# Kernel optimization log

Hardware: AMD Instinct MI355X
Metric: run time of the kernel (lower is better)

Reference implementation:

```python
import jax, jax.numpy as jnp
import numpy as np

TONECURVE_LENGTH = 256
RESOLUTION = 1024  # tone_curve_resolution
B, H, W = 8, 1024, 1536

RANGES = {
    'Temperature': (2000.0, 50000.0),
    'Tint': (-150.0, 150.0),
    'Exposure2012': (-5.0, 5.0),
    'Contrast2012': (-100.0, 100.0),
    'Highlights2012': (-100.0, 100.0),
    'Shadows2012': (-100.0, 100.0),
    'Whites2012': (-100.0, 100.0),
    'Blacks2012': (-100.0, 100.0),
    'Vibrance': (-100.0, 100.0),
    'Saturation': (-100.0, 100.0),
}

def _denorm(name, v):
    lo, hi = RANGES[name]
    return lo + 0.5 * (v + 1.0) * (hi - lo)

def _luminance(img):
    return 0.2126 * img[:, 0:1] + 0.7152 * img[:, 1:2] + 0.0722 * img[:, 2:3]

def _white_balance(img, temperature, tint):
    temp = jnp.clip(temperature, 2000.0, 50000.0)
    tr = 6500.0 / temp
    red = jnp.sqrt(tr)
    blue = 1.0 / jnp.sqrt(tr)
    ts = jnp.clip(tint / 150.0, -1.5, 1.5)
    green = 1.0 - 0.1 * ts
    red = red * (1.0 + 0.05 * ts)
    blue = blue * (1.0 - 0.05 * ts)
    gains = jnp.stack([red, green, blue], axis=1)[:, :, None, None]  # [B,3,1,1]
    balanced = img * gains
    norm = jnp.max(gains, axis=1, keepdims=True)
    return jnp.clip(balanced / jnp.maximum(norm, 1e-4), 0.0, 4.0)

def _region(img, luma, value, pivot, width):
    strength = (value / 100.0)[:, None, None, None]
    mask = jax.nn.sigmoid((luma - pivot) / width)
    mask = mask - jnp.mean(mask, axis=(2, 3), keepdims=True)
    new_luma = jnp.clip(luma + strength * mask, 0.0, 1.0)
    ratio = jnp.where(luma > 1e-4, new_luma / jnp.maximum(luma, 1e-4), 1.0)
    return jnp.clip(img * ratio, 0.0, 1.0), new_luma

def _tone_curve(img, tone_curve):
    luma = jnp.clip(_luminance(img), 0.0, 1.0)  # [B,1,H,W]
    # linear interp of [B,L] control points to [B,RESOLUTION], align_corners=True
    src = jnp.arange(RESOLUTION, dtype=jnp.float32) * ((TONECURVE_LENGTH - 1) / (RESOLUTION - 1))
    i0 = jnp.floor(src).astype(jnp.int32)
    i1 = jnp.minimum(i0 + 1, TONECURVE_LENGTH - 1)
    w = src - i0.astype(jnp.float32)
    curve = tone_curve[:, i0] * (1.0 - w) + tone_curve[:, i1] * w  # [B,RESOLUTION]
    coords = luma * (RESOLUTION - 1)
    idx_low = jnp.floor(coords).astype(jnp.int32)
    idx_high = jnp.minimum(idx_low + 1, RESOLUTION - 1)
    weight = coords - idx_low.astype(jnp.float32)
    b = img.shape[0]
    g_low = jnp.take_along_axis(curve, idx_low.reshape(b, -1), axis=1).reshape(luma.shape)
    g_high = jnp.take_along_axis(curve, idx_high.reshape(b, -1), axis=1).reshape(luma.shape)
    target = (1.0 - weight) * g_low + weight * g_high
    ratio = jnp.where(luma > 1e-5, target / jnp.maximum(luma, 1e-5), 1.0)
    return jnp.clip(img * ratio, 0.0, 1.0)

def _vibrance(img, vibrance):
    luma = _luminance(img)
    chroma = img - luma
    cn = jnp.sqrt(jnp.sum(chroma * chroma, axis=1, keepdims=True) + 1e-6)
    mask = jnp.exp(-4.0 * cn)
    gain = jnp.clip(1.0 + (vibrance / 100.0)[:, None, None, None] * mask, 0.2, 4.0)
    return jnp.clip(luma + chroma * gain, 0.0, 1.0)

def _saturation(img, saturation):
    luma = _luminance(img)
    chroma = img - luma
    gain = (1.0 + saturation / 100.0)[:, None, None, None]
    return jnp.clip(luma + chroma * gain, 0.0, 1.0)


def setup_inputs() -> dict:
    key = jax.random.key(0)
    ks = jax.random.split(key, 12)
    sliders = {}
    names = ['temperature_n', 'tint_n', 'exposure_n', 'contrast_n', 'highlights_n',
             'shadows_n', 'whites_n', 'blacks_n', 'vibrance_n', 'saturation_n']
    for i, n in enumerate(names):
        sliders[n] = jax.random.uniform(ks[i], (B,), jnp.float32, -1.0, 1.0)
    image = jax.random.uniform(ks[10], (B, 3, H, W), jnp.float32)
    tone_curve = jnp.sort(jax.random.uniform(ks[11], (B, TONECURVE_LENGTH), jnp.float32), axis=1)
    return {'image': image, 'tone_curve': tone_curve, **sliders}


def reference(image, tone_curve, temperature_n, tint_n, exposure_n, contrast_n,
              highlights_n, shadows_n, whites_n, blacks_n, vibrance_n, saturation_n):
    img = jnp.clip(image, 0.0, 1.0)
    temperature = _denorm('Temperature', temperature_n)
    tint = _denorm('Tint', tint_n)
    exposure = _denorm('Exposure2012', exposure_n)
    contrast = _denorm('Contrast2012', contrast_n)
    highlights = _denorm('Highlights2012', highlights_n)
    shadows = _denorm('Shadows2012', shadows_n)
    whites = _denorm('Whites2012', whites_n)
    blacks = _denorm('Blacks2012', blacks_n)
    vibrance = _denorm('Vibrance', vibrance_n)
    saturation = _denorm('Saturation', saturation_n)

    img = _white_balance(img, temperature, tint)
    img = img * jnp.power(2.0, exposure)[:, None, None, None]  # exposure
    img = jnp.clip(img, 0.0, 4.0)
    factor = (1.0 + contrast / 100.0)[:, None, None, None]      # contrast
    img = jnp.clip((img - 0.5) * factor + 0.5, 0.0, 1.0)

    luma = jnp.clip(_luminance(img), 0.0, 1.0)
    img, luma = _region(img, luma, highlights, 0.7, 0.1)
    img, luma = _region(img, luma, shadows, 0.3, 0.12)
    img, luma = _region(img, luma, whites, 0.9, 0.08)
    img, luma = _region(img, luma, blacks, 0.1, 0.08)

    img = _tone_curve(img, tone_curve)
    img = _vibrance(img, vibrance)
    img = _saturation(img, saturation)
    return jnp.clip(img, 0.0, 1.0)
```

## Files before the change

### kernel.cpp

```cpp
#include <hip/hip_runtime.h>
#include <math.h>

#define H_DIM 1024
#define W_DIM 1536
#define HW_PIX (H_DIM * W_DIM)
#define NBATCH 8
#define QPB (HW_PIX / 4)
#define RBPB 192
#define QPT_R (QPB / (RBPB * 256))
#define FQPT 4
#define FBPB (QPB / (256 * FQPT))
#define RESOLUTION 1024
#define TC_LEN 256

typedef float vfloat4 __attribute__((ext_vector_type(4)));

struct Sliders {
    const float* temperature; const float* tint; const float* exposure; const float* contrast;
    const float* highlights;  const float* shadows; const float* whites; const float* blacks;
    const float* vibrance;    const float* saturation;
};

__device__ __forceinline__ float denorm(float v, float lo, float hi) {
    return lo + 0.5f * (v + 1.0f) * (hi - lo);
}
__device__ __forceinline__ float clamp01(float x) {
    return __builtin_amdgcn_fmed3f(x, 0.f, 1.f);
}
__device__ __forceinline__ float clampf(float x, float lo, float hi) {
    return fminf(fmaxf(x, lo), hi);
}
__device__ __forceinline__ float sigmoidf(float x) {
    float t = __builtin_amdgcn_exp2f(x * -1.4426950408889634f);
    return __builtin_amdgcn_rcpf(1.0f + t);
}

struct FrontP { float sr, sg, sb, em, cf; };

__device__ __forceinline__ FrontP front_params(const Sliders& S, int b) {
    float temp = clampf(denorm(S.temperature[b], 2000.f, 50000.f), 2000.f, 50000.f);
    float tr   = 6500.f / temp;
    float red  = sqrtf(tr);
    float blue = 1.0f / sqrtf(tr);
    float ts   = clampf(denorm(S.tint[b], -150.f, 150.f) * (1.0f / 150.0f), -1.5f, 1.5f);
    float green = 1.0f - 0.1f * ts;
    red  *= (1.0f + 0.05f * ts);
    blue *= (1.0f - 0.05f * ts);
    float norm = fmaxf(fmaxf(red, green), blue);
    float inv  = 1.0f / fmaxf(norm, 1e-4f);
    FrontP p;
    p.sr = red * inv; p.sg = green * inv; p.sb = blue * inv;
    p.em = exp2f(denorm(S.exposure[b], -5.f, 5.f));
    p.cf = 1.0f + denorm(S.contrast[b], -100.f, 100.f) * 0.01f;
    return p;
}

__device__ __forceinline__ float front_chan(float x, float s, float em, float cf) {
    x = clamp01(x);
    x = x * s;
    x = fminf(x * em, 4.0f);
    return clamp01((x - 0.5f) * cf + 0.5f);
}

__device__ __forceinline__ float luminance(float r, float g, float b) {
    return 0.2126f * r + 0.7152f * g + 0.0722f * b;
}

__device__ __forceinline__ double block_sum_d(double v) {
    #pragma unroll
    for (int o = 32; o > 0; o >>= 1) v += __shfl_down(v, o, 64);
    __shared__ double s[4];
    int lane = threadIdx.x & 63, wid = threadIdx.x >> 6;
    if (lane == 0) s[wid] = v;
    __syncthreads();
    double r = 0.0;
    if (threadIdx.x == 0) r = s[0] + s[1] + s[2] + s[3];
    return r;
}

__device__ __forceinline__ float partial_mean(const double* __restrict__ ws_part, int k, int b) {
    const double* pp = ws_part + (k * NBATCH + b) * RBPB;
    double v = (threadIdx.x < RBPB) ? pp[threadIdx.x] : 0.0;
    double t = block_sum_d(v);
    __shared__ float sh;
    if (threadIdx.x == 0) sh = (float)(t * (1.0 / (double)HW_PIX));
    __syncthreads();
    float m = sh;
    __syncthreads();
    return m;
}

__device__ __forceinline__ void build_curve(float* curve, const float* tone_curve, int b) {
    const float* tc = tone_curve + b * TC_LEN;
    for (int j = threadIdx.x; j < RESOLUTION; j += 256) {
        float src = (float)j * ((float)(TC_LEN - 1) / (float)(RESOLUTION - 1));
        float fi  = floorf(src);
        int   i0  = (int)fi;
        int   i1  = min(i0 + 1, TC_LEN - 1);
        float w   = src - fi;
        curve[j]  = tc[i0] * (1.0f - w) + tc[i1] * w;
    }
}

template <int R, bool USE_LUMA>
__global__ __launch_bounds__(256)
void reduce_kernel(const float* __restrict__ image, Sliders S,
                   float* __restrict__ ws_luma, double* __restrict__ ws_part) {
    const int b   = blockIdx.x / RBPB;
    const int blk = blockIdx.x % RBPB;

    const float pivots[4] = {0.7f, 0.3f, 0.9f, 0.1f};
    const float invw[4]   = {1.0f / 0.1f, 1.0f / 0.12f, 1.0f / 0.08f, 1.0f / 0.08f};
    const float* sliders[4] = {S.highlights, S.shadows, S.whites, S.blacks};

    float strength[4], meanv[4];
    #pragma unroll
    for (int k = 0; k < R; k++) {
        strength[k] = denorm(sliders[k][b], -100.f, 100.f) * 0.01f;
        meanv[k]    = partial_mean(ws_part, k, b);
    }
    FrontP p = front_params(S, b);

    double sum = 0.0;
    #pragma unroll
    for (int it = 0; it < QPT_R; it++) {
        const int q   = blk * (256 * QPT_R) + it * 256 + threadIdx.x;
        const int off = q * 4;

        float4 L;
        if (USE_LUMA && R > 0) {
            L = *reinterpret_cast<const float4*>(ws_luma + (size_t)b * HW_PIX + off);
        } else {
            const float* base = image + (size_t)b * 3 * HW_PIX + off;
            float4 r4 = *reinterpret_cast<const float4*>(base);
            float4 g4 = *reinterpret_cast<const float4*>(base + HW_PIX);
            float4 b4 = *reinterpret_cast<const float4*>(base + 2 * HW_PIX);
            float* rr = reinterpret_cast<float*>(&r4);
            float* gg = reinterpret_cast<float*>(&g4);
            float* bb = reinterpret_cast<float*>(&b4);
            float* ll = reinterpret_cast<float*>(&L);
            #pragma unroll
            for (int i = 0; i < 4; i++) {
                float r  = front_chan(rr[i], p.sr, p.em, p.cf);
                float g  = front_chan(gg[i], p.sg, p.em, p.cf);
                float bl = front_chan(bb[i], p.sb, p.em, p.cf);
                ll[i] = clamp01(luminance(r, g, bl));
            }
            if (USE_LUMA && R == 0)
                *reinterpret_cast<float4*>(ws_luma + (size_t)b * HW_PIX + off) = L;
        }

        const float* ll = reinterpret_cast<const float*>(&L);
        #pragma unroll
        for (int i = 0; i < 4; i++) {
            float lum = ll[i];
            #pragma unroll
            for (int k = 0; k < R; k++) {
                float mask = sigmoidf((lum - pivots[k]) * invw[k]);
                lum = clamp01(lum + strength[k] * (mask - meanv[k]));
            }
            sum += (double)sigmoidf((lum - pivots[R]) * invw[R]);
        }
    }
    sum = block_sum_d(sum);
    if (threadIdx.x == 0) ws_part[(R * NBATCH + b) * RBPB + blk] = sum;
}

__global__ __launch_bounds__(256)
void final_kernel(const float* __restrict__ image, const float* __restrict__ tone_curve,
                  Sliders S, const double* __restrict__ ws_part, float* __restrict__ out) {
    const int b   = blockIdx.x / FBPB;
    const int blk = blockIdx.x % FBPB;

    __shared__ float curve[RESOLUTION];
    build_curve(curve, tone_curve, b);

    const float pivots[4] = {0.7f, 0.3f, 0.9f, 0.1f};
    const float invw[4]   = {1.0f / 0.1f, 1.0f / 0.12f, 1.0f / 0.08f, 1.0f / 0.08f};
    const float* sliders[4] = {S.highlights, S.shadows, S.whites, S.blacks};

    FrontP p = front_params(S, b);
    float strength[4], meanv[4];
    #pragma unroll
    for (int k = 0; k < 4; k++) {
        strength[k] = denorm(sliders[k][b], -100.f, 100.f) * 0.01f;
        meanv[k]    = partial_mean(ws_part, k, b);
    }
    float vib  = denorm(S.vibrance[b],   -100.f, 100.f) * 0.01f;
    float satg = 1.0f + denorm(S.saturation[b], -100.f, 100.f) * 0.01f;

    for (int it = 0; it < FQPT; it++) {
        const int q   = blk * (256 * FQPT) + it * 256 + threadIdx.x;
        const int off = q * 4;

        const float* base = image + (size_t)b * 3 * HW_PIX + off;
        float4 r4 = *reinterpret_cast<const float4*>(base);
        float4 g4 = *reinterpret_cast<const float4*>(base + HW_PIX);
        float4 b4 = *reinterpret_cast<const float4*>(base + 2 * HW_PIX);
        float* rr = reinterpret_cast<float*>(&r4);
        float* gg = reinterpret_cast<float*>(&g4);
        float* bb = reinterpret_cast<float*>(&b4);

        #pragma unroll
        for (int i = 0; i < 4; i++) {
            float r  = front_chan(rr[i], p.sr, p.em, p.cf);
            float g  = front_chan(gg[i], p.sg, p.em, p.cf);
            float bl = front_chan(bb[i], p.sb, p.em, p.cf);
            float lum = clamp01(luminance(r, g, bl));

            #pragma unroll
            for (int k = 0; k < 4; k++) {
                float mask = sigmoidf((lum - pivots[k]) * invw[k]);
                float nl   = clamp01(lum + strength[k] * (mask - meanv[k]));
                float ratio = (lum > 1e-4f) ? nl * __builtin_amdgcn_rcpf(lum) : 1.0f;
                r  = fminf(r * ratio, 1.f);
                g  = fminf(g * ratio, 1.f);
                bl = fminf(bl * ratio, 1.f);
                lum = nl;
            }

            float tl = clamp01(luminance(r, g, bl));
            float coords = tl * (float)(RESOLUTION - 1);
            float fidx = floorf(coords);
            int   i0 = (int)fidx;
            int   i1 = min(i0 + 1, RESOLUTION - 1);
            float w  = coords - fidx;
            float target = (1.0f - w) * curve[i0] + w * curve[i1];
            float ratio  = (tl > 1e-5f) ? target * __builtin_amdgcn_rcpf(tl) : 1.0f;
            r  = fminf(r * ratio, 1.f);
            g  = fminf(g * ratio, 1.f);
            bl = fminf(bl * ratio, 1.f);

            float l2 = luminance(r, g, bl);
            float cr = r - l2, cg = g - l2, cb = bl - l2;
            float cn = sqrtf(cr * cr + cg * cg + cb * cb + 1e-6f);
            float gmask = __builtin_amdgcn_exp2f(cn * -5.771f);
            float vg = __builtin_amdgcn_fmed3f(1.0f + vib * gmask, 0.2f, 4.0f);
            r  = clamp01(l2 + cr * vg);
            g  = clamp01(l2 + cg * vg);
            bl = clamp01(l2 + cb * vg);

            float l3 = luminance(r, g, bl);
            r  = clamp01(l3 + (r - l3) * satg);
            g  = clamp01(l3 + (g - l3) * satg);
            bl = clamp01(l3 + (bl - l3) * satg);

            rr[i] = r; gg[i] = g; bb[i] = bl;
        }

        float* op = out + (size_t)b * 3 * HW_PIX + off;
        __builtin_nontemporal_store(*reinterpret_cast<vfloat4*>(&r4),
                                    reinterpret_cast<vfloat4*>(op));
        __builtin_nontemporal_store(*reinterpret_cast<vfloat4*>(&g4),
                                    reinterpret_cast<vfloat4*>(op + HW_PIX));
        __builtin_nontemporal_store(*reinterpret_cast<vfloat4*>(&b4),
                                    reinterpret_cast<vfloat4*>(op + 2 * HW_PIX));
    }
}

extern "C" void kernel_launch(void* const* d_in, const int* in_sizes, int n_in,
                              void* d_out, int out_size, void* d_ws, size_t ws_size,
                              hipStream_t stream) {
    const float* image      = (const float*)d_in[0];
    const float* tone_curve = (const float*)d_in[1];
    Sliders S;
    S.temperature = (const float*)d_in[2];
    S.tint        = (const float*)d_in[3];
    S.exposure    = (const float*)d_in[4];
    S.contrast    = (const float*)d_in[5];
    S.highlights  = (const float*)d_in[6];
    S.shadows     = (const float*)d_in[7];
    S.whites      = (const float*)d_in[8];
    S.blacks      = (const float*)d_in[9];
    S.vibrance    = (const float*)d_in[10];
    S.saturation  = (const float*)d_in[11];
    float* out = (float*)d_out;

    double* ws_part = (double*)d_ws;
    float*  ws_luma = (float*)((char*)d_ws + 4 * NBATCH * RBPB * sizeof(double) + 256);
    bool use_luma = ws_size >= 4 * NBATCH * RBPB * sizeof(double) + 256
                              + (size_t)NBATCH * HW_PIX * sizeof(float);

    dim3 rgrid(NBATCH * RBPB), block(256);
    if (use_luma) {
        reduce_kernel<0, true><<<rgrid, block, 0, stream>>>(image, S, ws_luma, ws_part);
        reduce_kernel<1, true><<<rgrid, block, 0, stream>>>(image, S, ws_luma, ws_part);
        reduce_kernel<2, true><<<rgrid, block, 0, stream>>>(image, S, ws_luma, ws_part);
        reduce_kernel<3, true><<<rgrid, block, 0, stream>>>(image, S, ws_luma, ws_part);
    } else {
        reduce_kernel<0, false><<<rgrid, block, 0, stream>>>(image, S, ws_luma, ws_part);
        reduce_kernel<1, false><<<rgrid, block, 0, stream>>>(image, S, ws_luma, ws_part);
        reduce_kernel<2, false><<<rgrid, block, 0, stream>>>(image, S, ws_luma, ws_part);
        reduce_kernel<3, false><<<rgrid, block, 0, stream>>>(image, S, ws_luma, ws_part);
    }
    dim3 fgrid(NBATCH * FBPB);
    final_kernel<<<fgrid, block, 0, stream>>>(image, tone_curve, S, ws_part, out);
}
```

Before: 368.1 us.

## Fuse reduction passes and final pass into one persistent kernel with grid barriers

Measured after the change: 762.1 us. 2.07x slower.

```diff
diff --git a/kernel.cpp b/kernel.cpp
--- a/kernel.cpp
+++ b/kernel.cpp
@@ -6,14 +6,15 @@
 #define HW_PIX (H_DIM * W_DIM)
 #define NBATCH 8
 #define QPB (HW_PIX / 4)
-#define RBPB 192
-#define QPT_R (QPB / (RBPB * 256))
-#define FQPT 4
-#define FBPB (QPB / (256 * FQPT))
+#define BLKB 96
+#define NBLK (NBATCH * BLKB)
+#define QPT (QPB / (BLKB * 256))
 #define RESOLUTION 1024
 #define TC_LEN 256
+#define SPIN_CAP 300000
 
 typedef float vfloat4 __attribute__((ext_vector_type(4)));
+typedef unsigned long long u64;
 
 struct Sliders {
     const float* temperature; const float* tint; const float* exposure; const float* contrast;
@@ -78,18 +79,6 @@
     return r;
 }
 
-__device__ __forceinline__ float partial_mean(const double* __restrict__ ws_part, int k, int b) {
-    const double* pp = ws_part + (k * NBATCH + b) * RBPB;
-    double v = (threadIdx.x < RBPB) ? pp[threadIdx.x] : 0.0;
-    double t = block_sum_d(v);
-    __shared__ float sh;
-    if (threadIdx.x == 0) sh = (float)(t * (1.0 / (double)HW_PIX));
-    __syncthreads();
-    float m = sh;
-    __syncthreads();
-    return m;
-}
-
 __device__ __forceinline__ void build_curve(float* curve, const float* tone_curve, int b) {
     const float* tc = tone_curve + b * TC_LEN;
     for (int j = threadIdx.x; j < RESOLUTION; j += 256) {
@@ -102,110 +91,133 @@
     }
 }
 
-template <int R, bool USE_LUMA>
-__global__ __launch_bounds__(256)
-void reduce_kernel(const float* __restrict__ image, Sliders S,
-                   float* __restrict__ ws_luma, double* __restrict__ ws_part) {
-    const int b   = blockIdx.x / RBPB;
-    const int blk = blockIdx.x % RBPB;
+__device__ __forceinline__ float publish_mean(int slot, int phase, int b, int bb,
+                                              double acc, u64* part, unsigned int* ctr) {
+    double tot = block_sum_d(acc);
+    __shared__ float msh;
+    if (threadIdx.x == 0) {
+        u64 bits = __builtin_bit_cast(u64, tot);
+        __hip_atomic_store(&part[(slot * NBATCH + b) * BLKB + bb], bits,
+                           __ATOMIC_RELEASE, __HIP_MEMORY_SCOPE_AGENT);
+        __hip_atomic_fetch_add(ctr, 1u, __ATOMIC_ACQ_REL, __HIP_MEMORY_SCOPE_AGENT);
+        const unsigned int target = (unsigned int)(phase * NBLK);
+        int spins = 0;
+        while (__hip_atomic_load(ctr, __ATOMIC_ACQUIRE, __HIP_MEMORY_SCOPE_AGENT) < target) {
+            if (++spins > SPIN_CAP) break;
+        }
+    }
+    __syncthreads();
+    double v = 0.0;
+    if (threadIdx.x < BLKB) {
+        u64 bits = __hip_atomic_load(&part[(slot * NBATCH + b) * BLKB + threadIdx.x],
+                                     __ATOMIC_RELAXED, __HIP_MEMORY_SCOPE_AGENT);
+        v = __builtin_bit_cast(double, bits);
+    }
+    double t2 = block_sum_d(v);
+    if (threadIdx.x == 0) msh = (float)(t2 * (1.0 / (double)HW_PIX));
+    __syncthreads();
+    float m = msh;
+    __syncthreads();
+    return m;
+}
+
+template <int K>
+__device__ __forceinline__ double phaseB_acc(const unsigned short* __restrict__ lslice,
+                                             int bb, int tid,
+                                             const float* pivots, const float* invw,
+                                             const float* strength, const float* meanv) {
+    double acc = 0.0;
+    for (int it = 0; it < QPT; it++) {
+        const int off = (bb * (256 * QPT) + it * 256 + tid) * 4;
+        ushort4 lq = *reinterpret_cast<const ushort4*>(lslice + off);
+        const unsigned short* qs = reinterpret_cast<const unsigned short*>(&lq);
+        #pragma unroll
+        for (int i = 0; i < 4; i++) {
+            float l = (float)qs[i] * (1.0f / 65535.0f);
+            #pragma unroll
+            for (int j = 0; j < K; j++) {
+                float mask = sigmoidf((l - pivots[j]) * invw[j]);
+                l = clamp01(l + strength[j] * (mask - meanv[j]));
+            }
+            acc += (double)sigmoidf((l - pivots[K]) * invw[K]);
+        }
+    }
+    return acc;
+}
+
+__global__ __launch_bounds__(256, 4)
+void mega_kernel(const float* __restrict__ image, const float* __restrict__ tone_curve,
+                 Sliders S, unsigned int* __restrict__ ctr, u64* __restrict__ part,
+                 unsigned short* __restrict__ ws_luma, float* __restrict__ out)
+{
+    const int b   = blockIdx.x / BLKB;
+    const int bb  = blockIdx.x % BLKB;
+    const int tid = threadIdx.x;
+
+    __shared__ float curve[RESOLUTION];
+    build_curve(curve, tone_curve, b);
 
     const float pivots[4] = {0.7f, 0.3f, 0.9f, 0.1f};
     const float invw[4]   = {1.0f / 0.1f, 1.0f / 0.12f, 1.0f / 0.08f, 1.0f / 0.08f};
     const float* sliders[4] = {S.highlights, S.shadows, S.whites, S.blacks};
 
-    float strength[4], meanv[4];
+    FrontP p = front_params(S, b);
+    float strength[4];
     #pragma unroll
-    for (int k = 0; k < R; k++) {
+    for (int k = 0; k < 4; k++)
         strength[k] = denorm(sliders[k][b], -100.f, 100.f) * 0.01f;
-        meanv[k]    = partial_mean(ws_part, k, b);
-    }
-    FrontP p = front_params(S, b);
-
-    double sum = 0.0;
-    #pragma unroll
-    for (int it = 0; it < QPT_R; it++) {
-        const int q   = blk * (256 * QPT_R) + it * 256 + threadIdx.x;
-        const int off = q * 4;
-
-        float4 L;
-        if (USE_LUMA && R > 0) {
-            L = *reinterpret_cast<const float4*>(ws_luma + (size_t)b * HW_PIX + off);
-        } else {
-            const float* base = image + (size_t)b * 3 * HW_PIX + off;
-            float4 r4 = *reinterpret_cast<const float4*>(base);
-            float4 g4 = *reinterpret_cast<const float4*>(base + HW_PIX);
-            float4 b4 = *reinterpret_cast<const float4*>(base + 2 * HW_PIX);
-            float* rr = reinterpret_cast<float*>(&r4);
-            float* gg = reinterpret_cast<float*>(&g4);
-            float* bb = reinterpret_cast<float*>(&b4);
-            float* ll = reinterpret_cast<float*>(&L);
-            #pragma unroll
-            for (int i = 0; i < 4; i++) {
-                float r  = front_chan(rr[i], p.sr, p.em, p.cf);
-                float g  = front_chan(gg[i], p.sg, p.em, p.cf);
-                float bl = front_chan(bb[i], p.sb, p.em, p.cf);
-                ll[i] = clamp01(luminance(r, g, bl));
-            }
-            if (USE_LUMA && R == 0)
-                *reinterpret_cast<float4*>(ws_luma + (size_t)b * HW_PIX + off) = L;
-        }
-
-        const float* ll = reinterpret_cast<const float*>(&L);
+    float vib  = denorm(S.vibrance[b],   -100.f, 100.f) * 0.01f;
+    float satg = 1.0f + denorm(S.saturation[b], -100.f, 100.f) * 0.01f;
+
+    unsigned short* lslice = ws_luma + (size_t)b * HW_PIX;
+    const float* ibase = image + (size_t)b * 3 * HW_PIX;
+
+    double acc = 0.0;
+    for (int it = 0; it < QPT; it++) {
+        const int off = (bb * (256 * QPT) + it * 256 + tid) * 4;
+        float4 r4 = *reinterpret_cast<const float4*>(ibase + off);
+        float4 g4 = *reinterpret_cast<const float4*>(ibase + HW_PIX + off);
+        float4 b4 = *reinterpret_cast<const float4*>(ibase + 2 * HW_PIX + off);
+        const float* rr  = reinterpret_cast<const float*>(&r4);
+        const float* gg  = reinterpret_cast<const float*>(&g4);
+        const float* bb4 = reinterpret_cast<const float*>(&b4);
+        ushort4 pk;
+        unsigned short* pks = reinterpret_cast<unsigned short*>(&pk);
         #pragma unroll
         for (int i = 0; i < 4; i++) {
-            float lum = ll[i];
-            #pragma unroll
-            for (int k = 0; k < R; k++) {
-                float mask = sigmoidf((lum - pivots[k]) * invw[k]);
-                lum = clamp01(lum + strength[k] * (mask - meanv[k]));
-            }
-            sum += (double)sigmoidf((lum - pivots[R]) * invw[R]);
+            float r  = front_chan(rr[i],  p.sr, p.em, p.cf);
+            float g  = front_chan(gg[i],  p.sg, p.em, p.cf);
+            float bl = front_chan(bb4[i], p.sb, p.em, p.cf);
+            float l  = clamp01(luminance(r, g, bl));
+            acc += (double)sigmoidf((l - pivots[0]) * invw[0]);
+            pks[i] = (unsigned short)(l * 65535.0f + 0.5f);
         }
-    }
-    sum = block_sum_d(sum);
-    if (threadIdx.x == 0) ws_part[(R * NBATCH + b) * RBPB + blk] = sum;
-}
-
-__global__ __launch_bounds__(256)
-void final_kernel(const float* __restrict__ image, const float* __restrict__ tone_curve,
-                  Sliders S, const double* __restrict__ ws_part, float* __restrict__ out) {
-    const int b   = blockIdx.x / FBPB;
-    const int blk = blockIdx.x % FBPB;
-
-    __shared__ float curve[RESOLUTION];
-    build_curve(curve, tone_curve, b);
-
-    const float pivots[4] = {0.7f, 0.3f, 0.9f, 0.1f};
-    const float invw[4]   = {1.0f / 0.1f, 1.0f / 0.12f, 1.0f / 0.08f, 1.0f / 0.08f};
-    const float* sliders[4] = {S.highlights, S.shadows, S.whites, S.blacks};
-
-    FrontP p = front_params(S, b);
-    float strength[4], meanv[4];
-    #pragma unroll
-    for (int k = 0; k < 4; k++) {
-        strength[k] = denorm(sliders[k][b], -100.f, 100.f) * 0.01f;
-        meanv[k]    = partial_mean(ws_part, k, b);
-    }
-    float vib  = denorm(S.vibrance[b],   -100.f, 100.f) * 0.01f;
-    float satg = 1.0f + denorm(S.saturation[b], -100.f, 100.f) * 0.01f;
-
-    for (int it = 0; it < FQPT; it++) {
-        const int q   = blk * (256 * FQPT) + it * 256 + threadIdx.x;
-        const int off = q * 4;
-
-        const float* base = image + (size_t)b * 3 * HW_PIX + off;
-        float4 r4 = *reinterpret_cast<const float4*>(base);
-        float4 g4 = *reinterpret_cast<const float4*>(base + HW_PIX);
-        float4 b4 = *reinterpret_cast<const float4*>(base + 2 * HW_PIX);
-        float* rr = reinterpret_cast<float*>(&r4);
-        float* gg = reinterpret_cast<float*>(&g4);
-        float* bb = reinterpret_cast<float*>(&b4);
+        *reinterpret_cast<ushort4*>(lslice + off) = pk;
+    }
+
+    float meanv[4];
+    meanv[0] = publish_mean(0, 1, b, bb, acc, part, ctr);
+    meanv[1] = publish_mean(1, 2, b, bb,
+                 phaseB_acc<1>(lslice, bb, tid, pivots, invw, strength, meanv), part, ctr);
+    meanv[2] = publish_mean(2, 3, b, bb,
+                 phaseB_acc<2>(lslice, bb, tid, pivots, invw, strength, meanv), part, ctr);
+    meanv[3] = publish_mean(3, 4, b, bb,
+                 phaseB_acc<3>(lslice, bb, tid, pivots, invw, strength, meanv), part, ctr);
+
+    for (int it = 0; it < QPT; it++) {
+        const int off = (bb * (256 * QPT) + it * 256 + tid) * 4;
+        float4 r4 = *reinterpret_cast<const float4*>(ibase + off);
+        float4 g4 = *reinterpret_cast<const float4*>(ibase + HW_PIX + off);
+        float4 b4 = *reinterpret_cast<const float4*>(ibase + 2 * HW_PIX + off);
+        float* rr  = reinterpret_cast<float*>(&r4);
+        float* gg  = reinterpret_cast<float*>(&g4);
+        float* bb4 = reinterpret_cast<float*>(&b4);
 
         #pragma unroll
         for (int i = 0; i < 4; i++) {
-            float r  = front_chan(rr[i], p.sr, p.em, p.cf);
-            float g  = front_chan(gg[i], p.sg, p.em, p.cf);
-            float bl = front_chan(bb[i], p.sb, p.em, p.cf);
+            float r  = front_chan(rr[i],  p.sr, p.em, p.cf);
+            float g  = front_chan(gg[i],  p.sg, p.em, p.cf);
+            float bl = front_chan(bb4[i], p.sb, p.em, p.cf);
             float lum = clamp01(luminance(r, g, bl));
 
             #pragma unroll
@@ -245,7 +257,7 @@
             g  = clamp01(l3 + (g - l3) * satg);
             bl = clamp01(l3 + (bl - l3) * satg);
 
-            rr[i] = r; gg[i] = g; bb[i] = bl;
+            rr[i] = r; gg[i] = g; bb4[i] = bl;
         }
 
         float* op = out + (size_t)b * 3 * HW_PIX + off;
@@ -276,23 +288,13 @@
     S.saturation  = (const float*)d_in[11];
     float* out = (float*)d_out;
 
-    double* ws_part = (double*)d_ws;
-    float*  ws_luma = (float*)((char*)d_ws + 4 * NBATCH * RBPB * sizeof(double) + 256);
-    bool use_luma = ws_size >= 4 * NBATCH * RBPB * sizeof(double) + 256
-                              + (size_t)NBATCH * HW_PIX * sizeof(float);
-
-    dim3 rgrid(NBATCH * RBPB), block(256);
-    if (use_luma) {
-        reduce_kernel<0, true><<<rgrid, block, 0, stream>>>(image, S, ws_luma, ws_part);
-        reduce_kernel<1, true><<<rgrid, block, 0, stream>>>(image, S, ws_luma, ws_part);
-        reduce_kernel<2, true><<<rgrid, block, 0, stream>>>(image, S, ws_luma, ws_part);
-        reduce_kernel<3, true><<<rgrid, block, 0, stream>>>(image, S, ws_luma, ws_part);
-    } else {
-        reduce_kernel<0, false><<<rgrid, block, 0, stream>>>(image, S, ws_luma, ws_part);
-        reduce_kernel<1, false><<<rgrid, block, 0, stream>>>(image, S, ws_luma, ws_part);
-        reduce_kernel<2, false><<<rgrid, block, 0, stream>>>(image, S, ws_luma, ws_part);
-        reduce_kernel<3, false><<<rgrid, block, 0, stream>>>(image, S, ws_luma, ws_part);
-    }
-    dim3 fgrid(NBATCH * FBPB);
-    final_kernel<<<fgrid, block, 0, stream>>>(image, tone_curve, S, ws_part, out);
-}
+    unsigned int*   ctr     = (unsigned int*)d_ws;
+    u64*            part    = (u64*)((char*)d_ws + 256);
+    unsigned short* ws_luma = (unsigned short*)((char*)d_ws + 256
+                               + 4 * NBATCH * BLKB * sizeof(u64));
+
+    hipMemsetAsync(d_ws, 0, 256, stream);
+
+    mega_kernel<<<dim3(NBLK), dim3(256), 0, stream>>>(image, tone_curve, S,
+                                                      ctr, part, ws_luma, out);
+}
```
